# Kernel tuning notes

Measured on AMD Instinct MI355X. Metric: run time of the kernel, lower is better.

Reference implementation:

```python
import jax, jax.numpy as jnp
import numpy as np

B, S, D, H, L, W, O = 4, 1024, 512, 8, 6, 64, 300
DH = D // H          # head dim = 64
R = 2 * W + 3        # rel_proj output dim = 131
EPS = 1e-6


def setup_inputs() -> dict:
    key = jax.random.key(0)
    ks = jax.random.split(key, 12)
    sc = 0.02
    x = jax.random.normal(ks[0], (B, S, D), jnp.float32)
    inp = {
        "x": x,
        "ln1_g": jnp.ones((L, D), jnp.float32),
        "ln1_b": jnp.zeros((L, D), jnp.float32),
        "qkv_w": jax.random.normal(ks[1], (L, D, 3 * D), jnp.float32) * sc,
        "qkv_b": jnp.zeros((L, 3 * D), jnp.float32),
        "rel_w": jax.random.normal(ks[2], (DH, R), jnp.float32) * sc,
        "rel_b": jnp.zeros((R,), jnp.float32),
        "ln2_g": jnp.ones((L, D), jnp.float32),
        "ln2_b": jnp.zeros((L, D), jnp.float32),
        "mlp_w1": jax.random.normal(ks[3], (L, D, 4 * D), jnp.float32) * sc,
        "mlp_b1": jnp.zeros((L, 4 * D), jnp.float32),
        "mlp_w2": jax.random.normal(ks[4], (L, 4 * D, D), jnp.float32) * sc,
        "mlp_b2": jnp.zeros((L, D), jnp.float32),
        "normf_g": jnp.ones((D,), jnp.float32),
        "normf_b": jnp.zeros((D,), jnp.float32),
        "head_w": jax.random.normal(ks[5], (D, O), jnp.float32) * sc,
        "head_b": jnp.zeros((O,), jnp.float32),
        "mask": jax.random.randint(ks[6], (B, O), 0, 2, jnp.int32),
    }
    return inp


def _layernorm(x, g, b):
    m = jnp.mean(x, axis=-1, keepdims=True)
    v = jnp.mean(jnp.square(x - m), axis=-1, keepdims=True)
    return (x - m) * jax.lax.rsqrt(v + EPS) * g + b


def _forward(x, ln1_g, ln1_b, qkv_w, qkv_b, rel_w, rel_b, ln2_g, ln2_b,
             mlp_w1, mlp_b1, mlp_w2, mlp_b2, normf_g, normf_b, head_w, head_b, mask):
    b, s, d = x.shape
    # clamped relative offsets, shifted to [0, 2W]; shape [s, s]
    ar = jnp.arange(s)
    offsets = jnp.clip(ar[None, :] - ar[:, None], -W, W) + W
    off_bh = jnp.broadcast_to(offsets[None, None], (b, H, s, s))
    scale = 1.0 / np.sqrt(D / H)  # = 1/sqrt(dh)

    def block(xc, lp):
        (l1g, l1b, qw, qb, l2g, l2b, w1, b1, w2, b2) = lp
        h = _layernorm(xc, l1g, l1b)
        qkv = (h @ qw + qb).reshape(b, s, H, 3 * DH)
        q, k, v = jnp.split(qkv, 3, axis=-1)            # [b,s,h,dh] each
        q = q.transpose(0, 2, 1, 3)                     # [b,h,s,dh]
        k = k.transpose(0, 2, 1, 3)
        v = v.transpose(0, 2, 1, 3)
        content = jnp.einsum('bhik,bhjk->bhij', q, k) * scale
        pos = q @ rel_w + rel_b                          # [b,h,s,R]
        pos_scores = jnp.take_along_axis(pos, off_bh, axis=-1)  # [b,h,s,s]
        attn = jax.nn.softmax(content + pos_scores, axis=-1)
        out = jnp.einsum('bhij,bhjk->bhik', attn, v)     # [b,h,s,dh]
        xc = xc + out.transpose(0, 2, 1, 3).reshape(b, s, d)
        h2 = _layernorm(xc, l2g, l2b)
        m = jax.nn.gelu(h2 @ w1 + b1, approximate=False) @ w2 + b2
        return xc + m, None

    layer_params = (ln1_g, ln1_b, qkv_w, qkv_b, ln2_g, ln2_b,
                    mlp_w1, mlp_b1, mlp_w2, mlp_b2)
    x, _ = jax.lax.scan(block, x, layer_params)
    x = _layernorm(x, normf_g, normf_b)[:, 0, :]         # CLS token
    logits = x @ head_w + head_b                          # [b, O]
    return jnp.where(mask == 0, -jnp.inf, logits)


def reference(x, ln1_g, ln1_b, qkv_w, qkv_b, rel_w, rel_b, ln2_g, ln2_b,
              mlp_w1, mlp_b1, mlp_w2, mlp_b2, normf_g, normf_b, head_w, head_b, mask):
    return _forward(x, ln1_g, ln1_b, qkv_w, qkv_b, rel_w, rel_b, ln2_g, ln2_b,
                    mlp_w1, mlp_b1, mlp_w2, mlp_b2, normf_g, normf_b, head_w, head_b, mask)
```

## Files before the change

kernel.cpp:

```cpp
#include <hip/hip_runtime.h>
#include <math.h>

#define B_  4
#define S_  1024
#define D_  512
#define H_  8
#define L_  6
#define W_  64
#define O_  300
#define DH_ 64
#define R_  131
#define R2_ 132

typedef __attribute__((ext_vector_type(8))) short bf16x8;
typedef __attribute__((ext_vector_type(4))) float f32x4;

#define SWZ(r) ((((r) ^ ((r) >> 3)) & 7) << 4)

__device__ __forceinline__ float gelu_f(float x) {
    return 0.5f * x * (1.0f + erff(x * 0.70710678118654752f));
}

__device__ __forceinline__ unsigned short f2bf(float f) {
    union { float f; unsigned u; } c; c.f = f;
    unsigned u = c.u;
    unsigned r = (u + 0x7fffu + ((u >> 16) & 1u)) >> 16;
    return (unsigned short)r;
}
__device__ __forceinline__ float bf2f(unsigned short u) {
    union { unsigned u; float f; } c; c.u = ((unsigned)u) << 16; return c.f;
}

__device__ __forceinline__ void gload_lds16(const void* g, void* l) {
    __builtin_amdgcn_global_load_lds(
        (const __attribute__((address_space(1))) unsigned int*)g,
        (__attribute__((address_space(3))) unsigned int*)l, 16, 0, 0);
}

__global__ __launch_bounds__(256) void ln_kernel(
    const float* __restrict__ x, const float* __restrict__ g,
    const float* __restrict__ b, unsigned short* __restrict__ y, int rows)
{
    int wave = threadIdx.x >> 6;
    int lane = threadIdx.x & 63;
    int row  = blockIdx.x * 4 + wave;
    if (row >= rows) return;
    const float* xr = x + (size_t)row * D_;
    float4 v0 = *(const float4*)(xr + lane * 4);
    float4 v1 = *(const float4*)(xr + 256 + lane * 4);

    float s = v0.x + v0.y + v0.z + v0.w + v1.x + v1.y + v1.z + v1.w;
    #pragma unroll
    for (int off = 32; off >= 1; off >>= 1) s += __shfl_xor(s, off);
    float mean = s * (1.0f / 512.0f);

    float a0 = v0.x - mean, a1 = v0.y - mean, a2 = v0.z - mean, a3 = v0.w - mean;
    float a4 = v1.x - mean, a5 = v1.y - mean, a6 = v1.z - mean, a7 = v1.w - mean;
    float vs = a0*a0 + a1*a1 + a2*a2 + a3*a3 + a4*a4 + a5*a5 + a6*a6 + a7*a7;
    #pragma unroll
    for (int off = 32; off >= 1; off >>= 1) vs += __shfl_xor(vs, off);
    float rstd = rsqrtf(vs * (1.0f / 512.0f) + 1e-6f);

    float4 g0 = *(const float4*)(g + lane * 4);
    float4 g1 = *(const float4*)(g + 256 + lane * 4);
    float4 b0 = *(const float4*)(b + lane * 4);
    float4 b1 = *(const float4*)(b + 256 + lane * 4);

    unsigned short* yr = y + (size_t)row * D_;
    ushort4 p0 = {f2bf(a0 * rstd * g0.x + b0.x), f2bf(a1 * rstd * g0.y + b0.y),
                  f2bf(a2 * rstd * g0.z + b0.z), f2bf(a3 * rstd * g0.w + b0.w)};
    ushort4 p1 = {f2bf(a4 * rstd * g1.x + b1.x), f2bf(a5 * rstd * g1.y + b1.y),
                  f2bf(a6 * rstd * g1.z + b1.z), f2bf(a7 * rstd * g1.w + b1.w)};
    *(ushort4*)(yr + lane * 4)       = p0;
    *(ushort4*)(yr + 256 + lane * 4) = p1;
}

__global__ __launch_bounds__(256) void tconv_kernel(
    const float* __restrict__ in, unsigned short* __restrict__ out, int K, int N)
{
    __shared__ float t[32][33];
    int tx = threadIdx.x & 31, ty = threadIdx.x >> 5;
    int n0 = blockIdx.x * 32, k0 = blockIdx.y * 32;
    #pragma unroll
    for (int j = 0; j < 4; ++j)
        t[ty + 8*j][tx] = in[(size_t)(k0 + ty + 8*j) * N + n0 + tx];
    __syncthreads();
    #pragma unroll
    for (int j = 0; j < 4; ++j)
        out[(size_t)(n0 + ty + 8*j) * K + k0 + tx] = f2bf(t[tx][ty + 8*j]);
}

__global__ __launch_bounds__(256) void relw_prep(
    const float* __restrict__ rel_w, unsigned short* __restrict__ relwT)
{
    for (int i = threadIdx.x; i < 144 * 64; i += 256) {
        int r = i >> 6, c = i & 63;
        relwT[i] = (r < R_) ? f2bf(rel_w[(size_t)c * R_ + r]) : (unsigned short)0;
    }
}

__global__ __launch_bounds__(256) void prep_all(
    const float* __restrict__ qkv_w, const float* __restrict__ mlp_w1,
    const float* __restrict__ mlp_w2, const float* __restrict__ rel_w,
    unsigned short* __restrict__ wTq_all, unsigned short* __restrict__ wT1_all,
    unsigned short* __restrict__ wT2_all, unsigned short* __restrict__ relwT)
{
    int bid = blockIdx.x;
    if (bid >= 16896) {
        for (int i = threadIdx.x; i < 144 * 64; i += 256) {
            int r = i >> 6, c = i & 63;
            relwT[i] = (r < R_) ? f2bf(rel_w[(size_t)c * R_ + r]) : (unsigned short)0;
        }
        return;
    }
    int l = bid / 2816, rr = bid - l * 2816;
    const float* in; unsigned short* out; int K, N, bx, by;
    if (rr < 768) {
        in = qkv_w + (size_t)l * 512 * 1536; out = wTq_all + (size_t)l * 1536 * 512;
        K = 512; N = 1536; bx = rr % 48; by = rr / 48;
    } else if (rr < 1792) {
        int r2 = rr - 768;
        in = mlp_w1 + (size_t)l * 512 * 2048; out = wT1_all + (size_t)l * 2048 * 512;
        K = 512; N = 2048; bx = r2 % 64; by = r2 / 64;
    } else {
        int r2 = rr - 1792;
        in = mlp_w2 + (size_t)l * 2048 * 512; out = wT2_all + (size_t)l * 512 * 2048;
        K = 2048; N = 512; bx = r2 % 16; by = r2 / 16;
    }
    __shared__ float t[32][33];
    int tx = threadIdx.x & 31, ty = threadIdx.x >> 5;
    int n0 = bx * 32, k0 = by * 32;
    #pragma unroll
    for (int j = 0; j < 4; ++j)
        t[ty + 8*j][tx] = in[(size_t)(k0 + ty + 8*j) * N + n0 + tx];
    __syncthreads();
    #pragma unroll
    for (int j = 0; j < 4; ++j)
        out[(size_t)(n0 + ty + 8*j) * K + k0 + tx] = f2bf(t[tx][ty + 8*j]);
}

template<int ACT, int OBF, int BM, int BN, int WM, int WN, int BK>
__global__ __launch_bounds__(256) void mfma_gemm(
    const unsigned short* __restrict__ A, const unsigned short* __restrict__ BT,
    const float* __restrict__ bias, const float* __restrict__ resid,
    void* __restrict__ Cout, int M, int N, int K)
{
    static_assert(WM * WN == 4, "4 waves");
    constexpr int MFR = BM / WM / 16;
    constexpr int NFR = BN / WN / 16;
    constexpr int TPR = BK / 8;
    constexpr int RPP = 256 / TPR;
    constexpr int ACH = BM / RPP, BCH = BN / RPP;
    constexpr int LOADS = ACH + BCH;
    constexpr int KK = BK / 32;
    __shared__ __align__(16) unsigned short As[2 * BM * BK];
    __shared__ __align__(16) unsigned short Bs[2 * BN * BK];
    int tid  = threadIdx.x;
    int lane = tid & 63;
    int l15 = lane & 15, l4 = lane >> 4;
    int wid  = tid >> 6;
    int wave_m = (wid / WN) * (BM / WM);
    int wave_n = (wid % WN) * (BN / WN);

    int nwg = gridDim.x * gridDim.y;
    int bid0 = blockIdx.y * gridDim.x + blockIdx.x;
    int bid = (bid0 & 7) * (nwg >> 3) + (bid0 >> 3);
    int bm = (bid / gridDim.x) * BM, bn = (bid % gridDim.x) * BN;

    const f32x4 z4 = {0.f, 0.f, 0.f, 0.f};
    f32x4 acc[MFR][NFR];
    #pragma unroll
    for (int m = 0; m < MFR; ++m)
        #pragma unroll
        for (int n = 0; n < NFR; ++n) acc[m][n] = z4;

    int arow = tid / TPR;
    int acol8 = ((tid % TPR) ^ (arow & (TPR - 1))) * 8;
    const unsigned short* Ab = A  + (size_t)(bm + arow) * K + acol8;
    const unsigned short* Bb = BT + (size_t)(bn + arow) * K + acol8;
    unsigned short* Adst = As + tid * 8;
    unsigned short* Bdst = Bs + tid * 8;

    int swzA = l15 & (TPR - 1);
    const unsigned short* Afrag = As + (size_t)(wave_m + l15) * BK;
    const unsigned short* Bfrag = Bs + (size_t)(wave_n + l15) * BK;

    const int NT = K / BK;

    auto STAGE = [&](int buf, int k0) {
        #pragma unroll
        for (int ch = 0; ch < ACH; ++ch)
            gload_lds16(Ab + (size_t)ch * RPP * K + k0, Adst + buf * BM * BK + ch * RPP * BK);
        #pragma unroll
        for (int ch = 0; ch < BCH; ++ch)
            gload_lds16(Bb + (size_t)ch * RPP * K + k0, Bdst + buf * BN * BK + ch * RPP * BK);
    };

    STAGE(0, 0);
    STAGE(1, BK);

    int off8[KK];
    #pragma unroll
    for (int kk = 0; kk < KK; ++kk) off8[kk] = ((l4 + 4 * kk) ^ swzA) * 8;

    for (int t = 0; t < NT; ++t) {
        int cur = t & 1;
        if (t + 1 < NT) {
            if constexpr (LOADS == 6) asm volatile("s_waitcnt vmcnt(6)" ::: "memory");
            else if constexpr (LOADS == 4) asm volatile("s_waitcnt vmcnt(4)" ::: "memory");
            else asm volatile("s_waitcnt vmcnt(0)" ::: "memory");
        } else {
            asm volatile("s_waitcnt vmcnt(0)" ::: "memory");
        }
        __builtin_amdgcn_s_barrier();
        asm volatile("" ::: "memory");

        const unsigned short* Af = Afrag + cur * BM * BK;
        const unsigned short* Bf = Bfrag + cur * BN * BK;
        bf16x8 af[KK][MFR], bfr[KK][NFR];
        #pragma unroll
        for (int kk = 0; kk < KK; ++kk) {
            #pragma unroll
            for (int m = 0; m < MFR; ++m) af[kk][m]  = *(const bf16x8*)(Af + m * 16 * BK + off8[kk]);
            #pragma unroll
            for (int n = 0; n < NFR; ++n) bfr[kk][n] = *(const bf16x8*)(Bf + n * 16 * BK + off8[kk]);
        }
        asm volatile("s_waitcnt lgkmcnt(0)" ::: "memory");
        __builtin_amdgcn_sched_barrier(0);
        __builtin_amdgcn_s_barrier();
        asm volatile("" ::: "memory");

        if (t + 2 < NT) STAGE(cur, (t + 2) * BK);

        #pragma unroll
        for (int kk = 0; kk < KK; ++kk)
            #pragma unroll
            for (int m = 0; m < MFR; ++m)
                #pragma unroll
                for (int n = 0; n < NFR; ++n)
                    acc[m][n] = __builtin_amdgcn_mfma_f32_16x16x32_bf16(af[kk][m], bfr[kk][n], acc[m][n], 0, 0, 0);
    }

    int r0 = bm + wave_m + (l4 * 4);
    int c0 = bn + wave_n + l15;
    #pragma unroll
    for (int m = 0; m < MFR; ++m) {
        #pragma unroll
        for (int n = 0; n < NFR; ++n) {
            int c = c0 + n * 16;
            float bv = bias[c];
            #pragma unroll
            for (int q = 0; q < 4; ++q) {
                int r = r0 + m * 16 + q;
                float v = acc[m][n][q] + bv;
                if (ACT == 1) v = gelu_f(v);
                if (resid) v += resid[(size_t)r * N + c];
                if (OBF) ((unsigned short*)Cout)[(size_t)r * N + c] = f2bf(v);
                else     ((float*)Cout)[(size_t)r * N + c] = v;
            }
        }
    }
}

__global__ __launch_bounds__(512, 2) void attn_mfma(
    const unsigned short* __restrict__ qkv,
    const unsigned short* __restrict__ relwT,
    const float* __restrict__ rel_b,
    float* __restrict__ xres)
{
    __shared__ __align__(16) unsigned char shm[49664];
    unsigned char* Klds  = shm;
    unsigned char* Vtlds = shm + 16384;
    unsigned short* pos16 = (unsigned short*)(shm + 32768);
    float* mergeO  = (float*)shm;
    float* mergeML = (float*)(shm + 17408);

    int tid = threadIdx.x, lane = tid & 63, w = tid >> 6;
    int l15 = lane & 15, l4 = lane >> 4;
    int wq = w & 3;
    int g  = w >> 2;
    int it0 = blockIdx.x * 64;
    int h = blockIdx.y, b = blockIdx.z;
    const float LOG2E = 1.4426950408889634f;
    const float SC = 0.125f * LOG2E;
    const float THR = 11.5441f;

    bf16x8 qa[2];
    {
        const unsigned short* qp = qkv + (size_t)(b * S_ + it0 + wq * 16 + l15) * 1536 + h * 192 + l4 * 8;
        qa[0] = *(const bf16x8*)(qp);
        qa[1] = *(const bf16x8*)(qp + 32);
    }

    if (g == 0) {
        #pragma unroll
        for (int n = 0; n < 9; ++n) {
            f32x4 pacc = {0.f, 0.f, 0.f, 0.f};
            #pragma unroll
            for (int ks = 0; ks < 2; ++ks) {
                bf16x8 bv = *(const bf16x8*)(relwT + (size_t)(16 * n + l15) * 64 + ks * 32 + l4 * 8);
                pacc = __builtin_amdgcn_mfma_f32_16x16x32_bf16(qa[ks], bv, pacc, 0, 0, 0);
            }
            int c = 16 * n + l15;
            if (c < R_) {
                float rb = rel_b[c];
                #pragma unroll
                for (int q = 0; q < 4; ++q)
                    pos16[(wq * 16 + l4 * 4 + q) * R2_ + c] = f2bf((pacc[q] + rb) * LOG2E);
            }
        }
    }
    __syncthreads();

    int rloc = wq * 16 + l15;
    int i_glob = it0 + rloc;
    float p_lo = bf2f(pos16[rloc * R2_ + 0]);
    float p_hi = bf2f(pos16[rloc * R2_ + 128]);

    int rf = tid >> 2, seg = tid & 3;
    int gk = rf >> 6, rr = rf & 63;
    const unsigned short* kbase = qkv + (size_t)(b * S_ + gk * 512 + rr) * 1536 + h * 192 + 64 + seg * 16;
    int kbyt = gk * 8192 + ((rr * 128 + seg * 32) ^ SWZ(rr));
    int pf = tid >> 3, seg8 = tid & 7;
    int gv = pf >> 5, pp = pf & 31;
    const unsigned short* vbase = qkv + (size_t)(b * S_ + gv * 512 + 2 * pp) * 1536 + h * 192 + 128 + seg8 * 8;
    bf16x8 kr0, kr1, vr0, vr1;
    kr0 = *(const bf16x8*)(kbase);
    kr1 = *(const bf16x8*)(kbase + 8);
    vr0 = *(const bf16x8*)(vbase);
    vr1 = *(const bf16x8*)(vbase + 1536);

    const f32x4 z4 = {0.f, 0.f, 0.f, 0.f};
    f32x4 oacc[4];
    #pragma unroll
    for (int n = 0; n < 4; ++n) oacc[n] = z4;
    float mrun_s = -INFINITY, lrun_s = 0.f;
    int wmin = it0 + wq * 16;
    unsigned char* Kw = Klds + g * 8192;
    unsigned char* Vw = Vtlds + g * 8192;

    int idx_lo = (l15 + 32 * (l4 & 1)) * 4;
    int idx_hi = idx_lo + 64;
    bool hi_n = (l4 >> 1) != 0;

    for (int t = 0; t < 8; ++t) {
        int jt0 = g * 512 + t * 64;
        __syncthreads();
        *(bf16x8*)(Klds + kbyt) = kr0;
        *(bf16x8*)(Klds + (kbyt ^ 16)) = kr1;
        #pragma unroll
        for (int i = 0; i < 8; ++i) {
            int dh = seg8 * 8 + i;
            unsigned v01 = (unsigned)(unsigned short)vr0[i] | ((unsigned)(unsigned short)vr1[i] << 16);
            *(unsigned*)(Vtlds + gv * 8192 + ((dh * 128 + pp * 4) ^ SWZ(dh))) = v01;
        }
        __syncthreads();
        if (t < 7) {
            const unsigned short* kp = kbase + (size_t)(t + 1) * 64 * 1536;
            kr0 = *(const bf16x8*)(kp);
            kr1 = *(const bf16x8*)(kp + 8);
            const unsigned short* vp = vbase + (size_t)(t + 1) * 64 * 1536;
            vr0 = *(const bf16x8*)(vp);
            vr1 = *(const bf16x8*)(vp + 1536);
        }

        f32x4 ssw[4];
        #pragma unroll
        for (int n = 0; n < 4; ++n) ssw[n] = z4;
        #pragma unroll
        for (int n = 0; n < 4; ++n) {
            int kvr = 16 * n + l15;
            #pragma unroll
            for (int ks = 0; ks < 2; ++ks) {
                bf16x8 ak = *(const bf16x8*)(Kw + ((kvr * 128 + ks * 64 + l4 * 16) ^ SWZ(kvr)));
                ssw[n] = __builtin_amdgcn_mfma_f32_16x16x32_bf16(ak, qa[ks], ssw[n], 0, 0, 0);
            }
        }

        float sv[4][4];
        bool left  = (jt0 + 63 < wmin - 64);
        bool right = (jt0 > wmin + 15 + 64);
        if (left || right) {
            float pc = left ? p_lo : p_hi;
            #pragma unroll
            for (int n = 0; n < 4; ++n)
                #pragma unroll
                for (int r = 0; r < 4; ++r) sv[n][r] = fmaf(ssw[n][r], SC, pc);
        } else {
            #pragma unroll
            for (int n = 0; n < 4; ++n)
                #pragma unroll
                for (int r = 0; r < 4; ++r) {
                    int j = jt0 + 16 * n + l4 * 4 + r;
                    int off = j - i_glob;
                    off = off < -64 ? -64 : (off > 64 ? 64 : off);
                    sv[n][r] = fmaf(ssw[n][r], SC, bf2f(pos16[rloc * R2_ + off + 64]));
                }
        }

        float a0 = fmaxf(fmaxf(sv[0][0], sv[0][1]), fmaxf(sv[0][2], sv[0][3]));
        float a1 = fmaxf(fmaxf(sv[1][0], sv[1][1]), fmaxf(sv[1][2], sv[1][3]));
        float a2 = fmaxf(fmaxf(sv[2][0], sv[2][1]), fmaxf(sv[2][2], sv[2][3]));
        float a3 = fmaxf(fmaxf(sv[3][0], sv[3][1]), fmaxf(sv[3][2], sv[3][3]));
        float mx = fmaxf(fmaxf(a0, a1), fmaxf(a2, a3));
        mx = fmaxf(mx, __shfl_xor(mx, 16));
        mx = fmaxf(mx, __shfl_xor(mx, 32));
        if (!__all(mx - mrun_s <= THR)) {
            float mnew = fmaxf(mrun_s, mx);
            float al = exp2f(mrun_s - mnew);
            mrun_s = mnew;
            lrun_s *= al;
            float alv0 = __shfl(al, l4 * 4 + 0);
            float alv1 = __shfl(al, l4 * 4 + 1);
            float alv2 = __shfl(al, l4 * 4 + 2);
            float alv3 = __shfl(al, l4 * 4 + 3);
            #pragma unroll
            for (int n = 0; n < 4; ++n) {
                oacc[n][0] *= alv0; oacc[n][1] *= alv1;
                oacc[n][2] *= alv2; oacc[n][3] *= alv3;
            }
        }
        float rs = 0.f;
        #pragma unroll
        for (int n = 0; n < 4; ++n)
            #pragma unroll
            for (int r = 0; r < 4; ++r) {
                float p = exp2f(sv[n][r] - mrun_s);
                sv[n][r] = p;
                rs += p;
            }
        rs += __shfl_xor(rs, 16);
        rs += __shfl_xor(rs, 32);
        lrun_s += rs;

        unsigned pkk[4][2];
        #pragma unroll
        for (int n = 0; n < 4; ++n) {
            asm("v_cvt_pk_bf16_f32 %0, %1, %2" : "=v"(pkk[n][0]) : "v"(sv[n][0]), "v"(sv[n][1]));
            asm("v_cvt_pk_bf16_f32 %0, %1, %2" : "=v"(pkk[n][1]) : "v"(sv[n][2]), "v"(sv[n][3]));
        }
        bf16x8 pa[2];
        #pragma unroll
        for (int ks = 0; ks < 2; ++ks) {
            unsigned wrd[4];
            #pragma unroll
            for (int ww = 0; ww < 4; ++ww) {
                int srcidx = (ww >> 1) ? idx_hi : idx_lo;
                unsigned vlo = (unsigned)__builtin_amdgcn_ds_bpermute(srcidx, (int)pkk[2 * ks + 0][ww & 1]);
                unsigned vhi = (unsigned)__builtin_amdgcn_ds_bpermute(srcidx, (int)pkk[2 * ks + 1][ww & 1]);
                wrd[ww] = hi_n ? vhi : vlo;
            }
            union { unsigned u[4]; bf16x8 v; } cvt;
            cvt.u[0] = wrd[0]; cvt.u[1] = wrd[1]; cvt.u[2] = wrd[2]; cvt.u[3] = wrd[3];
            pa[ks] = cvt.v;
        }

        #pragma unroll
        for (int n = 0; n < 4; ++n) {
            int dh = 16 * n + l15;
            #pragma unroll
            for (int ks = 0; ks < 2; ++ks) {
                bf16x8 bv = *(const bf16x8*)(Vw + ((dh * 128 + ks * 64 + l4 * 16) ^ SWZ(dh)));
                oacc[n] = __builtin_amdgcn_mfma_f32_16x16x32_bf16(pa[ks], bv, oacc[n], 0, 0, 0);
            }
        }
    }

    __syncthreads();
    if (g == 1) {
        #pragma unroll
        for (int n = 0; n < 4; ++n)
            #pragma unroll
            for (int r = 0; r < 4; ++r)
                mergeO[(wq * 16 + l4 * 4 + r) * 68 + 16 * n + l15] = oacc[n][r];
        if (lane < 16) {
            mergeML[rloc * 2 + 0] = mrun_s;
            mergeML[rloc * 2 + 1] = lrun_s;
        }
    }
    __syncthreads();
    if (g == 0) {
        float mb = mergeML[rloc * 2 + 0];
        float lb = mergeML[rloc * 2 + 1];
        float M  = fmaxf(mrun_s, mb);
        float fa = exp2f(mrun_s - M);
        float fb = exp2f(mb - M);
        float inv = 1.0f / (lrun_s * fa + lb * fb);
        float A_s = fa * inv, B_s = fb * inv;
        float Av[4], Bv[4];
        #pragma unroll
        for (int r = 0; r < 4; ++r) {
            Av[r] = __shfl(A_s, l4 * 4 + r);
            Bv[r] = __shfl(B_s, l4 * 4 + r);
        }
        #pragma unroll
        for (int r = 0; r < 4; ++r) {
            int row = wq * 16 + l4 * 4 + r;
            float* xp = xres + (size_t)(b * S_ + it0 + row) * D_ + h * DH_;
            #pragma unroll
            for (int n = 0; n < 4; ++n)
                xp[16 * n + l15] += oacc[n][r] * Av[r] + mergeO[row * 68 + 16 * n + l15] * Bv[r];
        }
    }
}

__global__ __launch_bounds__(256) void head_kernel(
    const float* __restrict__ xc, const float* __restrict__ gf,
    const float* __restrict__ bfp, const float* __restrict__ hw,
    const float* __restrict__ hbias, const int* __restrict__ mask,
    float* __restrict__ out)
{
    __shared__ float a[4][512];
    __shared__ float part[4][64][4];
    int tid = threadIdx.x;
    int wv = tid >> 6, lane = tid & 63;
    {
        const float* xr = xc + (size_t)wv * S_ * D_;
        float4 v0 = *(const float4*)(xr + lane * 4);
        float4 v1 = *(const float4*)(xr + 256 + lane * 4);
        float s = v0.x + v0.y + v0.z + v0.w + v1.x + v1.y + v1.z + v1.w;
        #pragma unroll
        for (int off = 32; off >= 1; off >>= 1) s += __shfl_xor(s, off);
        float mean = s * (1.0f / 512.0f);
        float c0 = v0.x - mean, c1 = v0.y - mean, c2 = v0.z - mean, c3 = v0.w - mean;
        float c4 = v1.x - mean, c5 = v1.y - mean, c6 = v1.z - mean, c7 = v1.w - mean;
        float vs = c0*c0 + c1*c1 + c2*c2 + c3*c3 + c4*c4 + c5*c5 + c6*c6 + c7*c7;
        #pragma unroll
        for (int off = 32; off >= 1; off >>= 1) vs += __shfl_xor(vs, off);
        float rstd = rsqrtf(vs * (1.0f / 512.0f) + 1e-6f);
        float4 g0 = *(const float4*)(gf + lane * 4);
        float4 g1 = *(const float4*)(gf + 256 + lane * 4);
        float4 b0 = *(const float4*)(bfp + lane * 4);
        float4 b1 = *(const float4*)(bfp + 256 + lane * 4);
        a[wv][lane * 4 + 0] = c0 * rstd * g0.x + b0.x;
        a[wv][lane * 4 + 1] = c1 * rstd * g0.y + b0.y;
        a[wv][lane * 4 + 2] = c2 * rstd * g0.z + b0.z;
        a[wv][lane * 4 + 3] = c3 * rstd * g0.w + b0.w;
        a[wv][256 + lane * 4 + 0] = c4 * rstd * g1.x + b1.x;
        a[wv][256 + lane * 4 + 1] = c5 * rstd * g1.y + b1.y;
        a[wv][256 + lane * 4 + 2] = c6 * rstd * g1.z + b1.z;
        a[wv][256 + lane * 4 + 3] = c7 * rstd * g1.w + b1.w;
    }
    __syncthreads();

    int cl = tid & 63;
    int c  = blockIdx.x * 64 + cl;
    int ks = tid >> 6;
    float ac[4] = {0.f, 0.f, 0.f, 0.f};
    if (c < O_) {
        const float* wp = hw + (size_t)(ks * 128) * O_ + c;
        #pragma unroll 8
        for (int k = 0; k < 128; ++k) {
            float wvv = wp[(size_t)k * O_];
            int kk = ks * 128 + k;
            ac[0] = fmaf(a[0][kk], wvv, ac[0]);
            ac[1] = fmaf(a[1][kk], wvv, ac[1]);
            ac[2] = fmaf(a[2][kk], wvv, ac[2]);
            ac[3] = fmaf(a[3][kk], wvv, ac[3]);
        }
    }
    #pragma unroll
    for (int bb = 0; bb < 4; ++bb) part[ks][cl][bb] = ac[bb];
    __syncthreads();
    if (ks == 0 && c < O_) {
        float hbv = hbias[c];
        #pragma unroll
        for (int bb = 0; bb < 4; ++bb) {
            float v = part[0][cl][bb] + part[1][cl][bb] + part[2][cl][bb] + part[3][cl][bb] + hbv;
            out[bb * O_ + c] = (mask[bb * O_ + c] == 0) ? -1e30f : v;
        }
    }
}

extern "C" void kernel_launch(void* const* d_in, const int* in_sizes, int n_in,
                              void* d_out, int out_size, void* d_ws, size_t ws_size,
                              hipStream_t stream) {
    const float* x      = (const float*)d_in[0];
    const float* ln1_g  = (const float*)d_in[1];
    const float* ln1_b  = (const float*)d_in[2];
    const float* qkv_w  = (const float*)d_in[3];
    const float* qkv_b  = (const float*)d_in[4];
    const float* rel_w  = (const float*)d_in[5];
    const float* rel_b  = (const float*)d_in[6];
    const float* ln2_g  = (const float*)d_in[7];
    const float* ln2_b  = (const float*)d_in[8];
    const float* mlp_w1 = (const float*)d_in[9];
    const float* mlp_b1 = (const float*)d_in[10];
    const float* mlp_w2 = (const float*)d_in[11];
    const float* mlp_b2 = (const float*)d_in[12];
    const float* normf_g = (const float*)d_in[13];
    const float* normf_b = (const float*)d_in[14];
    const float* head_w  = (const float*)d_in[15];
    const float* head_b  = (const float*)d_in[16];
    const int*   mask    = (const int*)d_in[17];
    float* out = (float*)d_out;
    float* ws  = (float*)d_ws;

    const int NR = B_ * S_;
    dim3 blk(256);

    float* x_cur = ws;
    float* reg2  = ws + 2097152;
    unsigned short* qkv16 = (unsigned short*)reg2;
    unsigned short* midb  = (unsigned short*)reg2;

    hipMemcpyAsync(x_cur, x, (size_t)NR * D_ * sizeof(float),
                   hipMemcpyDeviceToDevice, stream);

    bool hoist = ws_size >= (size_t)15995392 * 4;

    if (hoist) {
        unsigned short* hb      = (unsigned short*)(ws + 6291456);
        unsigned short* wTq_all = (unsigned short*)(ws + 7340032);
        unsigned short* wT1_all = (unsigned short*)(ws + 9699328);
        unsigned short* wT2_all = (unsigned short*)(ws + 12845056);
        unsigned short* relwT   = (unsigned short*)(ws + 15990784);

        prep_all<<<16897, blk, 0, stream>>>(qkv_w, mlp_w1, mlp_w2, rel_w,
                                            wTq_all, wT1_all, wT2_all, relwT);

        for (int l = 0; l < L_; ++l) {
            ln_kernel<<<NR / 4, blk, 0, stream>>>(x_cur, ln1_g + l * D_, ln1_b + l * D_, hb, NR);
            mfma_gemm<0, 1, 128, 64, 4, 1, 64><<<dim3(24, 32), blk, 0, stream>>>(
                hb, wTq_all + (size_t)l * 1536 * 512, qkv_b + (size_t)l * 3 * D_,
                nullptr, qkv16, NR, 3 * D_, D_);
            attn_mfma<<<dim3(S_ / 64, H_, B_), dim3(512), 0, stream>>>(qkv16, relwT, rel_b, x_cur);
            ln_kernel<<<NR / 4, blk, 0, stream>>>(x_cur, ln2_g + l * D_, ln2_b + l * D_, hb, NR);
            mfma_gemm<1, 1, 128, 64, 4, 1, 64><<<dim3(32, 32), blk, 0, stream>>>(
                hb, wT1_all + (size_t)l * 2048 * 512, mlp_b1 + (size_t)l * 4 * D_,
                nullptr, midb, NR, 4 * D_, D_);
            mfma_gemm<0, 0, 64, 64, 2, 2, 64><<<dim3(8, 64), blk, 0, stream>>>(
                midb, wT2_all + (size_t)l * 512 * 2048, mlp_b2 + (size_t)l * D_,
                x_cur, x_cur, NR, D_, 4 * D_);
        }
        head_kernel<<<dim3(5), blk, 0, stream>>>(x_cur, normf_g, normf_b,
                                                 head_w, head_b, mask, out);
    } else {
        float* wregs = ws + 6291456;
        unsigned short* hb    = (unsigned short*)wregs;
        unsigned short* wTq   = (unsigned short*)(wregs + 1048576);
        unsigned short* wT1   = (unsigned short*)(wregs + 1441792);
        unsigned short* wT2   = (unsigned short*)(wregs + 1966080);
        unsigned short* relwT = (unsigned short*)(ws + 10616832);

        relw_prep<<<1, blk, 0, stream>>>(rel_w, relwT);
        for (int l = 0; l < L_; ++l) {
            ln_kernel<<<NR / 4, blk, 0, stream>>>(x_cur, ln1_g + l * D_, ln1_b + l * D_, hb, NR);
            tconv_kernel<<<dim3(48, 16), blk, 0, stream>>>(
                qkv_w + (size_t)l * D_ * 3 * D_, wTq, D_, 3 * D_);
            mfma_gemm<0, 1, 128, 64, 4, 1, 64><<<dim3(24, 32), blk, 0, stream>>>(
                hb, wTq, qkv_b + (size_t)l * 3 * D_, nullptr, qkv16, NR, 3 * D_, D_);
            attn_mfma<<<dim3(S_ / 64, H_, B_), dim3(512), 0, stream>>>(qkv16, relwT, rel_b, x_cur);
            ln_kernel<<<NR / 4, blk, 0, stream>>>(x_cur, ln2_g + l * D_, ln2_b + l * D_, hb, NR);
            tconv_kernel<<<dim3(64, 16), blk, 0, stream>>>(
                mlp_w1 + (size_t)l * D_ * 4 * D_, wT1, D_, 4 * D_);
            mfma_gemm<1, 1, 128, 64, 4, 1, 64><<<dim3(32, 32), blk, 0, stream>>>(
                hb, wT1, mlp_b1 + (size_t)l * 4 * D_, nullptr, midb, NR, 4 * D_, D_);
            tconv_kernel<<<dim3(16, 64), blk, 0, stream>>>(
                mlp_w2 + (size_t)l * 4 * D_ * D_, wT2, 4 * D_, D_);
            mfma_gemm<0, 0, 64, 64, 2, 2, 64><<<dim3(8, 64), blk, 0, stream>>>(
                midb, wT2, mlp_b2 + (size_t)l * D_, x_cur, x_cur, NR, D_, 4 * D_);
        }
        head_kernel<<<dim3(5), blk, 0, stream>>>(x_cur, normf_g, normf_b,
                                                 head_w, head_b, mask, out);
    }
}
```

Measured before the change: 624.5 us.

## Stage GEMM epilogue through LDS for vectorized stores and raise MFMA wave priority

The GEMM epilogue now writes bias/GELU results into the reused shared-memory buffer, then re-reads them so each thread issues 16-byte vector global stores and residual loads instead of scattered scalar accesses. The As/Bs buffers are merged into one smem array so the staging area can alias them. s_setprio brackets are also added around the MFMA loops in the GEMM and attention kernels to favour waves issuing matrix ops. The epilogue costs an extra barrier and LDS round trip, and the staging tile must fit in the freed buffer.

```diff
diff --git a/kernel.cpp b/kernel.cpp
--- a/kernel.cpp
+++ b/kernel.cpp
@@ -153,8 +153,9 @@
     constexpr int ACH = BM / RPP, BCH = BN / RPP;
     constexpr int LOADS = ACH + BCH;
     constexpr int KK = BK / 32;
-    __shared__ __align__(16) unsigned short As[2 * BM * BK];
-    __shared__ __align__(16) unsigned short Bs[2 * BN * BK];
+    __shared__ __align__(16) unsigned short smem[2 * (BM + BN) * BK];
+    unsigned short* As = smem;
+    unsigned short* Bs = smem + 2 * BM * BK;
     int tid  = threadIdx.x;
     int lane = tid & 63;
     int l15 = lane & 15, l4 = lane >> 4;
@@ -232,6 +233,7 @@
 
         if (t + 2 < NT) STAGE(cur, (t + 2) * BK);
 
+        __builtin_amdgcn_s_setprio(1);
         #pragma unroll
         for (int kk = 0; kk < KK; ++kk)
             #pragma unroll
@@ -239,25 +241,66 @@
                 #pragma unroll
                 for (int n = 0; n < NFR; ++n)
                     acc[m][n] = __builtin_amdgcn_mfma_f32_16x16x32_bf16(af[kk][m], bfr[kk][n], acc[m][n], 0, 0, 0);
-    }
-
-    int r0 = bm + wave_m + (l4 * 4);
-    int c0 = bn + wave_n + l15;
-    #pragma unroll
-    for (int m = 0; m < MFR; ++m) {
-        #pragma unroll
-        for (int n = 0; n < NFR; ++n) {
-            int c = c0 + n * 16;
-            float bv = bias[c];
-            #pragma unroll
-            for (int q = 0; q < 4; ++q) {
-                int r = r0 + m * 16 + q;
-                float v = acc[m][n][q] + bv;
-                if (ACT == 1) v = gelu_f(v);
-                if (resid) v += resid[(size_t)r * N + c];
-                if (OBF) ((unsigned short*)Cout)[(size_t)r * N + c] = f2bf(v);
-                else     ((float*)Cout)[(size_t)r * N + c] = v;
-            }
+        __builtin_amdgcn_s_setprio(0);
+    }
+
+    if constexpr (OBF) {
+        constexpr int STR = BN + 8;
+        unsigned short* st = smem;
+        #pragma unroll
+        for (int m = 0; m < MFR; ++m) {
+            #pragma unroll
+            for (int n = 0; n < NFR; ++n) {
+                int lc = wave_n + n * 16 + l15;
+                float bv = bias[bn + lc];
+                #pragma unroll
+                for (int q = 0; q < 4; ++q) {
+                    int lr = wave_m + m * 16 + l4 * 4 + q;
+                    float v = acc[m][n][q] + bv;
+                    if (ACT == 1) v = gelu_f(v);
+                    st[lr * STR + lc] = f2bf(v);
+                }
+            }
+        }
+        __syncthreads();
+        constexpr int PASS = BM * BN / (256 * 8);
+        #pragma unroll
+        for (int p = 0; p < PASS; ++p) {
+            int flat = (p * 256 + tid) * 8;
+            int row = flat / BN, col = flat % BN;
+            bf16x8 val = *(const bf16x8*)(st + row * STR + col);
+            *(bf16x8*)((unsigned short*)Cout + (size_t)(bm + row) * N + bn + col) = val;
+        }
+    } else {
+        constexpr int STR = BN + 4;
+        float* st = (float*)smem;
+        #pragma unroll
+        for (int m = 0; m < MFR; ++m) {
+            #pragma unroll
+            for (int n = 0; n < NFR; ++n) {
+                int lc = wave_n + n * 16 + l15;
+                float bv = bias[bn + lc];
+                #pragma unroll
+                for (int q = 0; q < 4; ++q) {
+                    int lr = wave_m + m * 16 + l4 * 4 + q;
+                    float v = acc[m][n][q] + bv;
+                    if (ACT == 1) v = gelu_f(v);
+                    st[lr * STR + lc] = v;
+                }
+            }
+        }
+        __syncthreads();
+        constexpr int PASS = BM * BN / (256 * 4);
+        #pragma unroll
+        for (int p = 0; p < PASS; ++p) {
+            int flat = (p * 256 + tid) * 4;
+            int row = flat / BN, col = flat % BN;
+            float4 val = *(const float4*)(st + row * STR + col);
+            if (resid) {
+                float4 rr = *(const float4*)(resid + (size_t)(bm + row) * N + bn + col);
+                val.x += rr.x; val.y += rr.y; val.z += rr.z; val.w += rr.w;
+            }
+            *(float4*)((float*)Cout + (size_t)(bm + row) * N + bn + col) = val;
         }
     }
 }
@@ -367,6 +410,7 @@
         f32x4 ssw[4];
         #pragma unroll
         for (int n = 0; n < 4; ++n) ssw[n] = z4;
+        __builtin_amdgcn_s_setprio(1);
         #pragma unroll
         for (int n = 0; n < 4; ++n) {
             int kvr = 16 * n + l15;
@@ -376,6 +420,7 @@
                 ssw[n] = __builtin_amdgcn_mfma_f32_16x16x32_bf16(ak, qa[ks], ssw[n], 0, 0, 0);
             }
         }
+        __builtin_amdgcn_s_setprio(0);
 
         float sv[4][4];
         bool left  = (jt0 + 63 < wmin - 64);
@@ -455,6 +500,7 @@
             pa[ks] = cvt.v;
         }
 
+        __builtin_amdgcn_s_setprio(1);
         #pragma unroll
         for (int n = 0; n < 4; ++n) {
             int dh = 16 * n + l15;
@@ -464,6 +510,7 @@
                 oacc[n] = __builtin_amdgcn_mfma_f32_16x16x32_bf16(pa[ks], bv, oacc[n], 0, 0, 0);
             }
         }
+        __builtin_amdgcn_s_setprio(0);
     }
 
     __syncthreads();
```

After: 582.8 us. 1.07x faster.
